# Kernel tuning notes

Hardware: AMD Instinct MI355X
Metric: run time of the kernel (lower is better)

The kernel has to match this reference:

```python
import jax, jax.numpy as jnp
import numpy as np


def setup_inputs() -> dict:
    key = jax.random.key(0)
    k1, k2 = jax.random.split(key)
    x = jax.random.normal(k1, (32, 3, 512, 512), dtype=jnp.float32)
    p = jax.random.uniform(k2, (32, 4), dtype=jnp.float32)
    return {"x": x, "p": p}


def _reflect(coord, size):
    # PyTorch grid_sample reflection padding, align_corners=False:
    # reflect about borders at -0.5 and size-0.5 (span = size), then clip.
    span = float(size)
    c = jnp.abs(coord + 0.5)
    flips = jnp.floor(c / span)
    extra = c - flips * span
    c = jnp.where(jnp.mod(flips, 2.0) == 0.0, extra, span - extra) - 0.5
    return jnp.clip(c, 0.0, size - 1.0)


def _bilinear_sample(img, ix, iy, W, H):
    # img: [C,H,W]; ix,iy: [H,W] pixel-space coords already reflected into [0,size-1]
    ix0f = jnp.floor(ix)
    iy0f = jnp.floor(iy)
    fx = ix - ix0f
    fy = iy - iy0f
    x0 = jnp.clip(ix0f.astype(jnp.int32), 0, W - 1)
    x1 = jnp.clip(ix0f.astype(jnp.int32) + 1, 0, W - 1)
    y0 = jnp.clip(iy0f.astype(jnp.int32), 0, H - 1)
    y1 = jnp.clip(iy0f.astype(jnp.int32) + 1, 0, H - 1)
    v00 = img[:, y0, x0]  # [C,H,W]
    v01 = img[:, y0, x1]
    v10 = img[:, y1, x0]
    v11 = img[:, y1, x1]
    return (v00 * (1.0 - fx) * (1.0 - fy)
            + v01 * fx * (1.0 - fy)
            + v10 * (1.0 - fx) * fy
            + v11 * fx * fy)


def reference(x, p):
    B, C, H, W = x.shape
    tx, ty, th, ts = p[:, 0], p[:, 1], p[:, 2], p[:, 3]
    c, s = jnp.cos(th), jnp.sin(th)
    # affine_grid base coords, align_corners=False: centers of pixels in [-1,1]
    xs = (jnp.arange(W, dtype=x.dtype) + 0.5) * (2.0 / W) - 1.0  # [W]
    ys = (jnp.arange(H, dtype=x.dtype) + 0.5) * (2.0 / H) - 1.0  # [H]
    a = (ts * c)[:, None, None]
    b = (-ts * s)[:, None, None]
    d = (ts * s)[:, None, None]
    e = (ts * c)[:, None, None]
    gx = a * xs[None, None, :] + b * ys[None, :, None] + tx[:, None, None]  # [B,H,W]
    gy = d * xs[None, None, :] + e * ys[None, :, None] + ty[:, None, None]  # [B,H,W]
    # unnormalize to pixel space (align_corners=False)
    ix = ((gx + 1.0) * W - 1.0) * 0.5
    iy = ((gy + 1.0) * H - 1.0) * 0.5
    ix = _reflect(ix, W)
    iy = _reflect(iy, H)
    out = jax.vmap(lambda img, jx, jy: _bilinear_sample(img, jx, jy, W, H))(x, ix, iy)
    return out
```

## Files before the change

### kernel.cpp

```cpp
#include <hip/hip_runtime.h>


#define B_ 32
#define C_ 3
#define H_ 512
#define W_ 512
#define TILE 32
#define LSTRIDE 60
#define SMEM_WORDS (57 * LSTRIDE + 64)

typedef float f32x4 __attribute__((ext_vector_type(4)));

__device__ __forceinline__ float reflect512(float coord) {
    const float c = fabsf(coord + 0.5f);
    const float m = c - floorf(c * (1.0f / 1024.0f)) * 1024.0f;
    const float t = 512.0f - fabsf(m - 512.0f);
    return fminf(fmaxf(t - 0.5f, 0.0f), 511.0f);
}

__global__ __launch_bounds__(256, 8)
void st_kernel(const float* __restrict__ x, const float* __restrict__ p,
               float* __restrict__ out) {
    __shared__ float smem[SMEM_WORDS];

    const int tid = threadIdx.x;

    const int bid = blockIdx.x;
    const int wid = (bid & 7) * 3072 + (bid >> 3);
    const int ch  = wid >> 13;
    const int rst = wid & 8191;
    const int b   = rst >> 8;
    const int til = rst & 255;
    const int tlx = til & 15;
    const int tly = til >> 4;

    const float tx = p[b * 4 + 0];
    const float ty = p[b * 4 + 1];
    const float th = p[b * 4 + 2];
    const float ts = p[b * 4 + 3];
    const float cth = __cosf(th), sth = __sinf(th);
    const float a  =  ts * cth;
    const float bb = -ts * sth;
    const float d  =  ts * sth;

    const float xs_c = ((float)(tlx * TILE) + 16.0f) * (2.0f / W_) - 1.0f;
    const float ys_c = ((float)(tly * TILE) + 16.0f) * (2.0f / H_) - 1.0f;
    const float gxc = a * xs_c + bb * ys_c + tx;
    const float gyc = d * xs_c + a  * ys_c + ty;
    const float rcx = reflect512(((gxc + 1.0f) * W_ - 1.0f) * 0.5f);
    const float rcy = reflect512(((gyc + 1.0f) * H_ - 1.0f) * 0.5f);
    const float ext = 16.0f * (fabsf(a) + fabsf(bb)) + 3.0f;

    int bx0 = max((int)floorf(rcx - ext), 0) & ~3;
    const int xhi = min((int)ceilf(rcx + ext) + 1, W_);
    int nw4 = (xhi - bx0 + 3) >> 2;
    nw4 = min(min(nw4, 15), (W_ - bx0) >> 2);

    int by0 = max((int)floorf(rcy - ext), 0);
    const int yhi = min((int)ceilf(rcy + ext) + 1, H_);
    const int nrows = min(yhi - by0, 57);

    const size_t plane = (size_t)H_ * W_;
    const float* img = x + ((size_t)b * C_ + ch) * plane;

    {
        const int c4 = tid & 15;
        const float* gp = img + (size_t)by0 * W_ + bx0;
        for (int r = tid >> 4; r < nrows; r += 16) {
            float* ld = &smem[r * LSTRIDE];
            if (c4 < nw4) {
                const f32x4 v = *reinterpret_cast<const f32x4*>(gp + (size_t)r * W_ + c4 * 4);
                *reinterpret_cast<f32x4*>(ld + c4 * 4) = v;
            } else if (c4 == nw4 && nw4 < 15) {
                *reinterpret_cast<f32x4*>(ld + c4 * 4) = (f32x4)(0.0f);
            }
        }
        if (tid < 16)
            *reinterpret_cast<f32x4*>(&smem[nrows * LSTRIDE + tid * 4]) = (f32x4)(0.0f);
    }
    __syncthreads();

    const int lr   = tid >> 3;
    const int lc   = (tid & 7) * 4;
    const int row  = tly * TILE + lr;
    const int col0 = tlx * TILE + lc;

    const float ysn = ((float)row  + 0.5f) * (2.0f / H_) - 1.0f;
    const float xsn = ((float)col0 + 0.5f) * (2.0f / W_) - 1.0f;
    float ix = ((a * xsn + bb * ysn + tx + 1.0f) * W_ - 1.0f) * 0.5f;
    float iy = ((d * xsn + a  * ysn + ty + 1.0f) * H_ - 1.0f) * 0.5f;

    const int koff = by0 * LSTRIDE + bx0;
    float acc[4];

    #pragma unroll
    for (int k = 0; k < 4; ++k) {
        const float rx  = reflect512(ix);
        const float ry  = reflect512(iy);
        const float x0f = floorf(rx);
        const float y0f = floorf(ry);
        const float fx  = rx - x0f;
        const float fy  = ry - y0f;
        const float ox  = 1.0f - fx;
        const float oy  = 1.0f - fy;
        const float w00 = ox * oy, w01 = fx * oy, w10 = ox * fy, w11 = fx * fy;

        const int idx = (int)y0f * LSTRIDE + (int)x0f - koff;
        const float* s = &smem[idx];
        acc[k] = s[0] * w00 + s[1] * w01
               + s[LSTRIDE] * w10 + s[LSTRIDE + 1] * w11;
        ix += a;
        iy += d;
    }

    float* o = out + ((size_t)b * C_ + ch) * plane + (size_t)row * W_ + col0;
    const f32x4 v = {acc[0], acc[1], acc[2], acc[3]};
    __builtin_nontemporal_store(v, reinterpret_cast<f32x4*>(o));
}

extern "C" void kernel_launch(void* const* d_in, const int* in_sizes, int n_in,
                              void* d_out, int out_size, void* d_ws, size_t ws_size,
                              hipStream_t stream) {
    const float* x = (const float*)d_in[0];
    const float* p = (const float*)d_in[1];
    float* out = (float*)d_out;

    dim3 block(256, 1, 1);
    dim3 grid((W_ / TILE) * (H_ / TILE) * B_ * C_, 1, 1);
    st_kernel<<<grid, block, 0, stream>>>(x, p, out);
}
```

Baseline: 186.1 us.

## Process all three channels per block with double-buffered LDS prefetch

Each block now handles one spatial tile across all three channels instead of one channel, so the affine, reflect and bilinear weight math is computed once and reused. The next channel's source window is loaded into registers while the current channel is sampled from LDS, then written into an alternate LDS buffer. This is meant to hide global load latency and remove redundant coordinate work. In exchange the grid is a third of the size, LDS use doubles, the occupancy hint drops from 8 to 5, and the row cap falls from 57 to 55, which could clip the window for large scales or rotations.

```diff
diff --git a/kernel.cpp b/kernel.cpp
--- a/kernel.cpp
+++ b/kernel.cpp
@@ -7,7 +7,8 @@
 #define W_ 512
 #define TILE 32
 #define LSTRIDE 60
-#define SMEM_WORDS (57 * LSTRIDE + 64)
+#define MAXROWS 55
+#define BUFW (MAXROWS * LSTRIDE + 64)
 
 typedef float f32x4 __attribute__((ext_vector_type(4)));
 
@@ -18,19 +19,17 @@
     return fminf(fmaxf(t - 0.5f, 0.0f), 511.0f);
 }
 
-__global__ __launch_bounds__(256, 8)
+__global__ __launch_bounds__(256, 5)
 void st_kernel(const float* __restrict__ x, const float* __restrict__ p,
                float* __restrict__ out) {
-    __shared__ float smem[SMEM_WORDS];
+    __shared__ float smem[2 * BUFW];
 
     const int tid = threadIdx.x;
 
     const int bid = blockIdx.x;
-    const int wid = (bid & 7) * 3072 + (bid >> 3);
-    const int ch  = wid >> 13;
-    const int rst = wid & 8191;
-    const int b   = rst >> 8;
-    const int til = rst & 255;
+    const int wid = (bid & 7) * 1024 + (bid >> 3);
+    const int b   = wid >> 8;
+    const int til = wid & 255;
     const int tlx = til & 15;
     const int tly = til >> 4;
 
@@ -58,27 +57,31 @@
 
     int by0 = max((int)floorf(rcy - ext), 0);
     const int yhi = min((int)ceilf(rcy + ext) + 1, H_);
-    const int nrows = min(yhi - by0, 57);
+    const int nrows = min(yhi - by0, MAXROWS);
 
     const size_t plane = (size_t)H_ * W_;
-    const float* img = x + ((size_t)b * C_ + ch) * plane;
+    const float* img = x + (size_t)b * C_ * plane;
+    const size_t gbase = (size_t)by0 * W_ + bx0;
+    const int c4 = tid & 15;
+    const int r0 = tid >> 4;
 
     {
-        const int c4 = tid & 15;
-        const float* gp = img + (size_t)by0 * W_ + bx0;
-        for (int r = tid >> 4; r < nrows; r += 16) {
-            float* ld = &smem[r * LSTRIDE];
-            if (c4 < nw4) {
-                const f32x4 v = *reinterpret_cast<const f32x4*>(gp + (size_t)r * W_ + c4 * 4);
-                *reinterpret_cast<f32x4*>(ld + c4 * 4) = v;
-            } else if (c4 == nw4 && nw4 < 15) {
-                *reinterpret_cast<f32x4*>(ld + c4 * 4) = (f32x4)(0.0f);
-            }
+        const float* gp = img + gbase;
+        for (int r = r0; r < nrows; r += 16)
+            if (c4 < nw4)
+                *reinterpret_cast<f32x4*>(&smem[r * LSTRIDE + c4 * 4]) =
+                    *reinterpret_cast<const f32x4*>(gp + (size_t)r * W_ + c4 * 4);
+        if (nw4 < 15)
+            for (int r = r0; r < nrows; r += 16)
+                if (c4 == nw4) {
+                    *reinterpret_cast<f32x4*>(&smem[r * LSTRIDE + c4 * 4]) = (f32x4)(0.0f);
+                    *reinterpret_cast<f32x4*>(&smem[BUFW + r * LSTRIDE + c4 * 4]) = (f32x4)(0.0f);
+                }
+        if (tid < 16) {
+            *reinterpret_cast<f32x4*>(&smem[nrows * LSTRIDE + tid * 4]) = (f32x4)(0.0f);
+            *reinterpret_cast<f32x4*>(&smem[BUFW + nrows * LSTRIDE + tid * 4]) = (f32x4)(0.0f);
         }
-        if (tid < 16)
-            *reinterpret_cast<f32x4*>(&smem[nrows * LSTRIDE + tid * 4]) = (f32x4)(0.0f);
     }
-    __syncthreads();
 
     const int lr   = tid >> 3;
     const int lc   = (tid & 7) * 4;
@@ -91,8 +94,8 @@
     float iy = ((d * xsn + a  * ysn + ty + 1.0f) * H_ - 1.0f) * 0.5f;
 
     const int koff = by0 * LSTRIDE + bx0;
-    float acc[4];
-
+    int   idx4[4];
+    float w00_[4], w01_[4], w10_[4], w11_[4];
     #pragma unroll
     for (int k = 0; k < 4; ++k) {
         const float rx  = reflect512(ix);
@@ -103,19 +106,58 @@
         const float fy  = ry - y0f;
         const float ox  = 1.0f - fx;
         const float oy  = 1.0f - fy;
-        const float w00 = ox * oy, w01 = fx * oy, w10 = ox * fy, w11 = fx * fy;
-
-        const int idx = (int)y0f * LSTRIDE + (int)x0f - koff;
-        const float* s = &smem[idx];
-        acc[k] = s[0] * w00 + s[1] * w01
-               + s[LSTRIDE] * w10 + s[LSTRIDE + 1] * w11;
+        w00_[k] = ox * oy; w01_[k] = fx * oy; w10_[k] = ox * fy; w11_[k] = fx * fy;
+        idx4[k] = (int)y0f * LSTRIDE + (int)x0f - koff;
         ix += a;
         iy += d;
     }
 
-    float* o = out + ((size_t)b * C_ + ch) * plane + (size_t)row * W_ + col0;
-    const f32x4 v = {acc[0], acc[1], acc[2], acc[3]};
-    __builtin_nontemporal_store(v, reinterpret_cast<f32x4*>(o));
+    float* outp = out + (size_t)b * C_ * plane + (size_t)row * W_ + col0;
+
+    f32x4 vr[4];
+    auto load_regs = [&](int ch) {
+        const float* gp = img + (size_t)ch * plane + gbase;
+        #pragma unroll
+        for (int i = 0; i < 4; ++i) {
+            const int rr = min(r0 + i * 16, nrows - 1);
+            vr[i] = (c4 < nw4)
+                ? *reinterpret_cast<const f32x4*>(gp + (size_t)rr * W_ + c4 * 4)
+                : (f32x4)(0.0f);
+        }
+    };
+    auto write_regs = [&](float* base) {
+        #pragma unroll
+        for (int i = 0; i < 4; ++i) {
+            const int r = r0 + i * 16;
+            if (r < nrows && c4 < nw4)
+                *reinterpret_cast<f32x4*>(base + r * LSTRIDE + c4 * 4) = vr[i];
+        }
+    };
+    auto compute_store = [&](int ch, const float* base) {
+        float acc[4];
+        #pragma unroll
+        for (int k = 0; k < 4; ++k) {
+            const float* s = base + idx4[k];
+            acc[k] = s[0] * w00_[k] + s[1] * w01_[k]
+                   + s[LSTRIDE] * w10_[k] + s[LSTRIDE + 1] * w11_[k];
+        }
+        const f32x4 v = {acc[0], acc[1], acc[2], acc[3]};
+        __builtin_nontemporal_store(v, reinterpret_cast<f32x4*>(outp + (size_t)ch * plane));
+    };
+
+    __syncthreads();
+
+    load_regs(1);
+    compute_store(0, smem);
+    write_regs(smem + BUFW);
+    __syncthreads();
+
+    load_regs(2);
+    compute_store(1, smem + BUFW);
+    write_regs(smem);
+    __syncthreads();
+
+    compute_store(2, smem);
 }
 
 extern "C" void kernel_launch(void* const* d_in, const int* in_sizes, int n_in,
@@ -126,6 +168,6 @@
     float* out = (float*)d_out;
 
     dim3 block(256, 1, 1);
-    dim3 grid((W_ / TILE) * (H_ / TILE) * B_ * C_, 1, 1);
+    dim3 grid((W_ / TILE) * (H_ / TILE) * B_, 1, 1);
     st_kernel<<<grid, block, 0, stream>>>(x, p, out);
 }
```

Result: no change. 186.7 us (+0.3%).
